# Kernel optimization log

Measured on AMD Instinct MI355X. Metric: run time of the kernel, lower is better.

The kernel has to match this reference:

```python
import jax, jax.numpy as jnp
import numpy as np

STATE_DIM = 256
ACTION_DIM = 2
HIDDEN = 512
N_HEADS = 5          # per ensemble; 2*N_HEADS stacked critics total
CEM_POP = 4096
CEM_ITERS = 4
ELITE_N = max(1, int(round(CEM_POP * 0.2)))  # 819
ACTION_LOW, ACTION_HIGH = -1.0, 1.0
INIT_STD, MIN_STD = 0.4, 0.1


def setup_inputs() -> dict:
    key = jax.random.key(0)
    ks = jax.random.split(key, 6)
    in_dim = STATE_DIM + ACTION_DIM
    state = jax.random.normal(ks[0], (1, STATE_DIM), dtype=jnp.float32)
    noise = jax.random.normal(ks[1], (CEM_ITERS, CEM_POP, ACTION_DIM), dtype=jnp.float32)
    W1 = jax.random.normal(ks[2], (2 * N_HEADS, in_dim, HIDDEN), dtype=jnp.float32) / np.sqrt(in_dim).astype(np.float32)
    b1 = jnp.zeros((2 * N_HEADS, HIDDEN), dtype=jnp.float32)
    W2 = jax.random.normal(ks[3], (2 * N_HEADS, HIDDEN, HIDDEN), dtype=jnp.float32) / np.sqrt(HIDDEN).astype(np.float32)
    b2 = jnp.zeros((2 * N_HEADS, HIDDEN), dtype=jnp.float32)
    W3 = jax.random.normal(ks[4], (2 * N_HEADS, HIDDEN, 1), dtype=jnp.float32) / np.sqrt(HIDDEN).astype(np.float32)
    b3 = jnp.zeros((2 * N_HEADS, 1), dtype=jnp.float32)
    return {"state": state, "noise": noise, "W1": W1, "b1": b1, "W2": W2, "b2": b2, "W3": W3, "b3": b3}


def _ensemble_scores(s_batch, a, W1, b1, W2, b2, W3, b3):
    # x: [P, state+action]; heads stacked on leading dim h = 2*N_HEADS
    x = jnp.concatenate([s_batch, a], axis=-1)
    h = jax.nn.relu(jnp.einsum('pi,hij->hpj', x, W1) + b1[:, None, :])
    h = jax.nn.relu(jnp.einsum('hpj,hjk->hpk', h, W2) + b2[:, None, :])
    q = (jnp.einsum('hpk,hko->hpo', h, W3) + b3[:, None, :])[..., 0]  # [2H, P]
    q1, q2 = q[:N_HEADS], q[N_HEADS:]
    return jnp.minimum(q1, q2).mean(axis=0)  # [P]


def reference(state, noise, W1, b1, W2, b2, W3, b3):
    s = state[0]  # squeeze(0)
    s_batch = jnp.broadcast_to(s, (CEM_POP, STATE_DIM))

    def step(carry, eps):
        mu, std, best_a, best_score = carry
        a = jnp.clip(mu + std * eps, ACTION_LOW, ACTION_HIGH)  # [P, A]
        scores = _ensemble_scores(s_batch, a, W1, b1, W2, b2, W3, b3)
        vals, idx = jax.lax.top_k(scores, ELITE_N)
        elite = a[idx]  # [ELITE_N, A]
        mu2 = elite.mean(axis=0)
        std2 = jnp.maximum(jnp.std(elite, axis=0, ddof=1), MIN_STD)  # torch unbiased std
        better = vals[0] > best_score
        best_a2 = jnp.where(better, elite[0], best_a)
        best_score2 = jnp.where(better, vals[0], best_score)
        return (mu2, std2, best_a2, best_score2), None

    carry0 = (jnp.zeros((ACTION_DIM,), jnp.float32),
              jnp.full((ACTION_DIM,), INIT_STD, jnp.float32),
              jnp.zeros((ACTION_DIM,), jnp.float32),
              jnp.float32(-jnp.inf))
    (mu, std, best_a, best_score), _ = jax.lax.scan(step, carry0, noise)
    return best_a[None, :]  # [1, ACTION_DIM]
```

## Files before the change

kernel.cpp:

```cpp
#include <hip/hip_runtime.h>
#include <math.h>

#define SDIM   256
#define HID    512
#define NH     5
#define HEADS  10
#define POP    4096
#define ITERS  4
#define ELITE  819
#define INIT_STDF 0.4f
#define MIN_STDF  0.1f

#define WS_BASE1 0
#define WS_Q     5120
#define WS_STATE 87040
#define WS_W2S_BYTE 348224
#define W2S_USHORTS (HEADS * 2 * 16 * 16384)
#define WS_NEED_BYTES (WS_W2S_BYTE + (size_t)W2S_USHORTS * 2)

typedef __attribute__((ext_vector_type(4))) float f32x4;
typedef __attribute__((ext_vector_type(8))) short bf16x8;

static __device__ __forceinline__ unsigned short bf16_rne(float x) {
    unsigned b = __float_as_uint(x);
    return (unsigned short)((b + 0x7FFFu + ((b >> 16) & 1u)) >> 16);
}

static __device__ __forceinline__ unsigned pack2(float x, float y) {
    unsigned r;
    asm("v_cvt_pk_bf16_f32 %0, %1, %2" : "=v"(r) : "v"(x), "v"(y));
    return r;
}

static __device__ __forceinline__ float clip1(float x) {
    return fminf(fmaxf(x, -1.f), 1.f);
}

__global__ __launch_bounds__(256) void k_base(const float* __restrict__ state,
                                              const float* __restrict__ W1,
                                              const float* __restrict__ b1,
                                              float* __restrict__ ws)
{
    const int h = blockIdx.y;
    const int j = blockIdx.x * 256 + threadIdx.x;
    const float* w1h = W1 + (size_t)h * 258 * HID;
    float acc = b1[h * HID + j];
    for (int i = 0; i < SDIM; ++i)
        acc += state[i] * w1h[(size_t)i * HID + j];
    ws[WS_BASE1 + h * HID + j] = acc;

    if (h == 0 && blockIdx.x == 0 && threadIdx.x == 0) {
        float* st = ws + WS_STATE;
        st[0] = 0.f; st[1] = 0.f;
        st[2] = INIT_STDF; st[3] = INIT_STDF;
        st[4] = 0.f; st[5] = 0.f;
        st[6] = -3.402823466e38f;
    }
}

__global__ __launch_bounds__(256) void k_split(const float* __restrict__ W2,
                                               unsigned short* __restrict__ W2S)
{
    const int h = blockIdx.z, cb = blockIdx.y, jc = blockIdx.x;
    const int c = threadIdx.x;
    unsigned short* slab = W2S + (size_t)((h * 2 + cb) * 16 + jc) * 16384;
    #pragma unroll
    for (int jg = 0; jg < 4; ++jg) {
        unsigned hp[4], lp[4];
        #pragma unroll
        for (int i = 0; i < 4; ++i) {
            const int j = jc * 32 + jg * 8 + 2 * i;
            float v0 = W2[(size_t)(h * HID + j) * HID + cb * 256 + c];
            float v1 = W2[(size_t)(h * HID + j + 1) * HID + cb * 256 + c];
            unsigned short h0 = bf16_rne(v0), h1 = bf16_rne(v1);
            float f0 = __uint_as_float((unsigned)h0 << 16);
            float f1 = __uint_as_float((unsigned)h1 << 16);
            unsigned short l0 = bf16_rne(v0 - f0), l1 = bf16_rne(v1 - f1);
            hp[i] = (unsigned)h0 | ((unsigned)h1 << 16);
            lp[i] = (unsigned)l0 | ((unsigned)l1 << 16);
        }
        uint4 HV, LV;
        HV.x = hp[0]; HV.y = hp[1]; HV.z = hp[2]; HV.w = hp[3];
        LV.x = lp[0]; LV.y = lp[1]; LV.z = lp[2]; LV.w = lp[3];
        *(uint4*)&slab[jg * 2048 + c * 8] = HV;
        *(uint4*)&slab[8192 + jg * 2048 + c * 8] = LV;
    }
}

__global__ __launch_bounds__(512, 4) void k_score_mfma10(
    const float* __restrict__ noise, const float* __restrict__ W1,
    const unsigned short* __restrict__ W2S,
    const float* __restrict__ b2, const float* __restrict__ W3,
    float* __restrict__ ws, int t)
{
    __shared__ unsigned short As[2][4096];
    __shared__ float red[8][64];

    const int tid = threadIdx.x;
    const int bid = blockIdx.x;
    const int w = (bid & 7) * 160 + (bid >> 3);
    const int h = w >> 7;
    const int rem = w & 127;
    const int cb = rem >> 6;
    const int rs = rem & 63;

    const int lane = tid & 63;
    const int wv = tid >> 6;
    const int l15 = lane & 15, lk = lane >> 4;

    const int arow = tid & 63;
    const int akg = (tid >> 6) & 3;
    const int ahalf = tid >> 8;

    const float* st = ws + WS_STATE;
    const float mu0 = st[0], mu1 = st[1], sd0 = st[2], sd1 = st[3];
    float2 e = *(const float2*)&noise[((size_t)t * POP + rs * 64 + arow) * 2];
    const float a0 = clip1(mu0 + sd0 * e.x);
    const float a1 = clip1(mu1 + sd1 * e.y);

    const float* base1 = ws + WS_BASE1 + h * HID;
    const float* w1u = W1 + ((size_t)h * 258 + 256) * HID;
    const float* w1v = W1 + ((size_t)h * 258 + 257) * HID;
    const unsigned short* bslab = W2S + (size_t)((h * 2 + cb) * 16) * 16384;
    const int bco = lk * 2048 + (wv * 32 + l15) * 8;

    auto computeA = [&](int jc, int buf) {
        const int j = jc * 32 + akg * 8 + ahalf * 4;
        f32x4 b0 = *(const f32x4*)&base1[j];
        f32x4 u0 = *(const f32x4*)&w1u[j];
        f32x4 v0 = *(const f32x4*)&w1v[j];
        float hv[4];
        #pragma unroll
        for (int i = 0; i < 4; ++i)
            hv[i] = fmaxf(b0[i] + a0 * u0[i] + a1 * v0[i], 0.f);
        unsigned ph[2], pl[2];
        #pragma unroll
        for (int i = 0; i < 2; ++i) {
            ph[i] = pack2(hv[2 * i], hv[2 * i + 1]);
            float fx = __uint_as_float(ph[i] << 16);
            float fy = __uint_as_float(ph[i] & 0xFFFF0000u);
            pl[i] = pack2(hv[2 * i] - fx, hv[2 * i + 1] - fy);
        }
        uint2 HV, LV;
        HV.x = ph[0]; HV.y = ph[1];
        LV.x = pl[0]; LV.y = pl[1];
        const int ao = akg * 512 + arow * 8 + ahalf * 4;
        *(uint2*)&As[buf][ao] = HV;
        *(uint2*)&As[buf][2048 + ao] = LV;
    };

    f32x4 acc[4][2];
    #pragma unroll
    for (int m = 0; m < 4; ++m)
        #pragma unroll
        for (int n = 0; n < 2; ++n)
            acc[m][n] = (f32x4){0.f, 0.f, 0.f, 0.f};

    computeA(0, 0);
    bf16x8 BH[2], BL[2];
    #pragma unroll
    for (int n = 0; n < 2; ++n) {
        BH[n] = *(const bf16x8*)(bslab + bco + n * 128);
        BL[n] = *(const bf16x8*)(bslab + 8192 + bco + n * 128);
    }
    __syncthreads();

    int cur = 0;
    #pragma unroll 1
    for (int kc = 0; kc < 16; ++kc) {
        bf16x8 AH[4], AL[4];
        #pragma unroll
        for (int m = 0; m < 4; ++m) {
            const int ad = lk * 512 + (m * 16 + l15) * 8;
            AH[m] = *(const bf16x8*)&As[cur][ad];
            AL[m] = *(const bf16x8*)&As[cur][2048 + ad];
        }
        const int nc = (kc < 15) ? kc + 1 : 15;
        const unsigned short* bnc = bslab + (size_t)nc * 16384;
        bf16x8 nBH[2], nBL[2];
        #pragma unroll
        for (int n = 0; n < 2; ++n) {
            nBH[n] = *(const bf16x8*)(bnc + bco + n * 128);
            nBL[n] = *(const bf16x8*)(bnc + 8192 + bco + n * 128);
        }
        __builtin_amdgcn_s_setprio(1);
        #pragma unroll
        for (int m = 0; m < 4; ++m)
            #pragma unroll
            for (int n = 0; n < 2; ++n)
                acc[m][n] = __builtin_amdgcn_mfma_f32_16x16x32_bf16(
                    AH[m], BH[n], acc[m][n], 0, 0, 0);
        #pragma unroll
        for (int m = 0; m < 4; ++m)
            #pragma unroll
            for (int n = 0; n < 2; ++n)
                acc[m][n] = __builtin_amdgcn_mfma_f32_16x16x32_bf16(
                    AL[m], BH[n], acc[m][n], 0, 0, 0);
        #pragma unroll
        for (int m = 0; m < 4; ++m)
            #pragma unroll
            for (int n = 0; n < 2; ++n)
                acc[m][n] = __builtin_amdgcn_mfma_f32_16x16x32_bf16(
                    AH[m], BL[n], acc[m][n], 0, 0, 0);
        __builtin_amdgcn_s_setprio(0);
        computeA(nc, cur ^ 1);
        __syncthreads();
        #pragma unroll
        for (int n = 0; n < 2; ++n) { BH[n] = nBH[n]; BL[n] = nBL[n]; }
        cur ^= 1;
    }

    float qp[4][4];
    #pragma unroll
    for (int m = 0; m < 4; ++m)
        #pragma unroll
        for (int r = 0; r < 4; ++r) qp[m][r] = 0.f;
    #pragma unroll
    for (int n = 0; n < 2; ++n) {
        int gcol = cb * 256 + wv * 32 + n * 16 + l15;
        float b2v = b2[h * HID + gcol];
        float w3v = W3[h * HID + gcol];
        #pragma unroll
        for (int m = 0; m < 4; ++m)
            #pragma unroll
            for (int r = 0; r < 4; ++r)
                qp[m][r] += fmaxf(acc[m][n][r] + b2v, 0.f) * w3v;
    }
    #pragma unroll
    for (int m = 0; m < 4; ++m)
        #pragma unroll
        for (int r = 0; r < 4; ++r) {
            float v = qp[m][r];
            v += __shfl_xor(v, 1);
            v += __shfl_xor(v, 2);
            v += __shfl_xor(v, 4);
            v += __shfl_xor(v, 8);
            if (l15 == 0) red[wv][m * 16 + lk * 4 + r] = v;
        }
    __syncthreads();
    if (tid < 64) {
        float q = 0.f;
        #pragma unroll
        for (int s = 0; s < 8; ++s) q += red[s][tid];
        ws[WS_Q + (size_t)(cb * HEADS + h) * POP + rs * 64 + tid] = q;
    }
}

__global__ __launch_bounds__(256) void k_score(const float* __restrict__ noise,
                                               const float* __restrict__ W1,
                                               const float* __restrict__ W2,
                                               const float* __restrict__ b2,
                                               const float* __restrict__ W3,
                                               float* __restrict__ ws, int t)
{
    __shared__ float h1[32][HID];
    __shared__ float a0s[32], a1s[32];
    __shared__ float red[2][16][2];

    const int tid = threadIdx.x;
    const int h   = blockIdx.y;
    const int p0  = blockIdx.x * 32;

    if (tid < 32) {
        const float* st = ws + WS_STATE;
        const int p = p0 + tid;
        float e0 = noise[((size_t)t * POP + p) * 2 + 0];
        float e1 = noise[((size_t)t * POP + p) * 2 + 1];
        a0s[tid] = fminf(fmaxf(st[0] + st[2] * e0, -1.f), 1.f);
        a1s[tid] = fminf(fmaxf(st[1] + st[3] * e1, -1.f), 1.f);
    }
    __syncthreads();

    const float* base1 = ws + WS_BASE1 + h * HID;
    const float* w1u = W1 + ((size_t)h * 258 + 256) * HID;
    const float* w1v = W1 + ((size_t)h * 258 + 257) * HID;
    #pragma unroll
    for (int jj = 0; jj < 2; ++jj) {
        int j = tid + jj * 256;
        float bb = base1[j], uu = w1u[j], vv = w1v[j];
        #pragma unroll
        for (int p = 0; p < 32; ++p)
            h1[p][j] = fmaxf(bb + a0s[p] * uu + a1s[p] * vv, 0.f);
    }
    __syncthreads();

    const int pg = tid >> 7;
    const int kl = tid & 127;
    const float* W2h = W2 + (size_t)h * HID * HID + kl;

    float acc[16][4];
    #pragma unroll
    for (int p = 0; p < 16; ++p)
        #pragma unroll
        for (int dk = 0; dk < 4; ++dk) acc[p][dk] = 0.f;

    for (int j0 = 0; j0 < HID; j0 += 4) {
        float w[4][4];
        #pragma unroll
        for (int dj = 0; dj < 4; ++dj)
            #pragma unroll
            for (int dk = 0; dk < 4; ++dk)
                w[dj][dk] = W2h[(size_t)(j0 + dj) * HID + dk * 128];
        #pragma unroll
        for (int p = 0; p < 16; ++p) {
            const float4 hv = *(const float4*)&h1[pg * 16 + p][j0];
            #pragma unroll
            for (int dk = 0; dk < 4; ++dk)
                acc[p][dk] += hv.x * w[0][dk] + hv.y * w[1][dk]
                            + hv.z * w[2][dk] + hv.w * w[3][dk];
        }
    }

    float b2v[4], w3v[4];
    #pragma unroll
    for (int dk = 0; dk < 4; ++dk) {
        b2v[dk] = b2[h * HID + kl + dk * 128];
        w3v[dk] = W3[h * HID + kl + dk * 128];
    }
    const int wid  = tid >> 6;
    const int lane = tid & 63;
    const int wig  = wid & 1;
    #pragma unroll
    for (int p = 0; p < 16; ++p) {
        float v = 0.f;
        #pragma unroll
        for (int dk = 0; dk < 4; ++dk)
            v += fmaxf(acc[p][dk] + b2v[dk], 0.f) * w3v[dk];
        #pragma unroll
        for (int off = 32; off; off >>= 1) v += __shfl_down(v, off);
        if (lane == 0) red[pg][p][wig] = v;
    }
    __syncthreads();
    if (tid < 32) {
        int pp = tid & 15, g = tid >> 4;
        ws[WS_Q + (size_t)h * POP + p0 + g * 16 + pp] =
            red[g][pp][0] + red[g][pp][1];
        ws[WS_Q + (size_t)(HEADS + h) * POP + p0 + g * 16 + pp] = 0.f;
    }
}

__global__ __launch_bounds__(1024) void k_select(const float* __restrict__ noise,
                                                 const float* __restrict__ b3,
                                                 float* __restrict__ ws,
                                                 float* __restrict__ out, int t)
{
    __shared__ float    sc[POP];
    __shared__ unsigned uk[POP];
    __shared__ unsigned hist[256];
    __shared__ int      scan2[1024];
    __shared__ float    rf[1024];
    __shared__ int      ri_[1024];
    __shared__ double   rd[1024];
    __shared__ unsigned s_prefix;
    __shared__ int      s_r;

    const int tid = threadIdx.x;
    const float* q = ws + WS_Q;
    float* st = ws + WS_STATE;
    const float mu0 = st[0], mu1 = st[1], sd0 = st[2], sd1 = st[3];

    {
        const int p = tid * 4;
        f32x4 s = (f32x4){0.f, 0.f, 0.f, 0.f};
        #pragma unroll
        for (int hh = 0; hh < NH; ++hh) {
            f32x4 qa0 = *(const f32x4*)&q[(size_t)hh * POP + p];
            f32x4 qa1 = *(const f32x4*)&q[(size_t)(HEADS + hh) * POP + p];
            f32x4 qb0 = *(const f32x4*)&q[(size_t)(NH + hh) * POP + p];
            f32x4 qb1 = *(const f32x4*)&q[(size_t)(HEADS + NH + hh) * POP + p];
            float ba = b3[hh], bb = b3[NH + hh];
            #pragma unroll
            for (int i = 0; i < 4; ++i)
                s[i] += fminf(qa0[i] + qa1[i] + ba, qb0[i] + qb1[i] + bb);
        }
        #pragma unroll
        for (int i = 0; i < 4; ++i) {
            float v = s[i] * 0.2f;
            sc[p + i] = v;
            unsigned b = __float_as_uint(v);
            uk[p + i] = (b & 0x80000000u) ? ~b : (b | 0x80000000u);
        }
    }
    __syncthreads();

    float mv = -3.402823466e38f; int mi = 0;
    #pragma unroll
    for (int k = 0; k < 4; ++k) {
        const int p = tid * 4 + k;
        float v = sc[p];
        if (v > mv) { mv = v; mi = p; }
    }
    rf[tid] = mv; ri_[tid] = mi;
    __syncthreads();
    for (int off = 512; off; off >>= 1) {
        if (tid < off) {
            float ov = rf[tid + off]; int oi = ri_[tid + off];
            if (ov > rf[tid] || (ov == rf[tid] && oi < ri_[tid])) {
                rf[tid] = ov; ri_[tid] = oi;
            }
        }
        __syncthreads();
    }
    const float maxsc = rf[0];
    const int argmax = ri_[0];
    __syncthreads();

    unsigned prefix = 0; int r = ELITE;
    for (int shift = 24; shift >= 0; shift -= 8) {
        if (tid < 256) hist[tid] = 0;
        __syncthreads();
        const unsigned himask = (shift < 24) ? (0xFFFFFFFFu << (shift + 8)) : 0u;
        for (int p = tid; p < POP; p += 1024) {
            unsigned key = uk[p];
            if ((key & himask) == prefix)
                atomicAdd(&hist[(key >> shift) & 255u], 1u);
        }
        __syncthreads();
        scan2[tid] = (tid < 256) ? (int)hist[tid] : 0;
        __syncthreads();
        for (int off = 1; off < 256; off <<= 1) {
            int v = (tid < 256 && tid + off < 256) ? scan2[tid + off] : 0;
            __syncthreads();
            if (tid < 256) scan2[tid] += v;
            __syncthreads();
        }
        if (tid < 256) {
            int above = (tid < 255) ? scan2[tid + 1] : 0;
            if (scan2[tid] >= r && above < r) {
                s_prefix = prefix | ((unsigned)tid << shift);
                s_r = r - above;
            }
        }
        __syncthreads();
        prefix = s_prefix; r = s_r;
        __syncthreads();
    }
    const unsigned uT = prefix;
    const int take = r;

    int tieloc = 0;
    {
        const int base = tid * 4;
        #pragma unroll
        for (int k = 0; k < 4; ++k) if (uk[base + k] == uT) tieloc++;
    }
    scan2[tid] = tieloc;
    __syncthreads();
    for (int off = 1; off < 1024; off <<= 1) {
        int v = (tid >= off) ? scan2[tid - off] : 0;
        __syncthreads();
        scan2[tid] += v;
        __syncthreads();
    }
    const int tieExcl = scan2[tid] - tieloc;

    double s0 = 0, s1 = 0, ss0 = 0, ss1 = 0;
    {
        const int base = tid * 4;
        int trank = tieExcl;
        #pragma unroll
        for (int k = 0; k < 4; ++k) {
            const int p = base + k;
            const unsigned key = uk[p];
            bool inc = false;
            if (key > uT) inc = true;
            else if (key == uT) { if (trank < take) inc = true; trank++; }
            if (inc) {
                float e0 = noise[((size_t)t * POP + p) * 2 + 0];
                float e1 = noise[((size_t)t * POP + p) * 2 + 1];
                float a0 = fminf(fmaxf(mu0 + sd0 * e0, -1.f), 1.f);
                float a1 = fminf(fmaxf(mu1 + sd1 * e1, -1.f), 1.f);
                s0 += a0; s1 += a1;
                ss0 += (double)a0 * a0; ss1 += (double)a1 * a1;
            }
        }
    }
    double S0, S1, SS0, SS1;
    rd[tid] = s0;  __syncthreads();
    for (int off = 512; off; off >>= 1) { if (tid < off) rd[tid] += rd[tid + off]; __syncthreads(); }
    S0 = rd[0]; __syncthreads();
    rd[tid] = s1;  __syncthreads();
    for (int off = 512; off; off >>= 1) { if (tid < off) rd[tid] += rd[tid + off]; __syncthreads(); }
    S1 = rd[0]; __syncthreads();
    rd[tid] = ss0; __syncthreads();
    for (int off = 512; off; off >>= 1) { if (tid < off) rd[tid] += rd[tid + off]; __syncthreads(); }
    SS0 = rd[0]; __syncthreads();
    rd[tid] = ss1; __syncthreads();
    for (int off = 512; off; off >>= 1) { if (tid < off) rd[tid] += rd[tid + off]; __syncthreads(); }
    SS1 = rd[0]; __syncthreads();

    if (tid == 0) {
        const double n = (double)ELITE;
        double m0 = S0 / n, m1 = S1 / n;
        double v0 = (SS0 - S0 * S0 / n) / (n - 1.0);
        double v1 = (SS1 - S1 * S1 / n) / (n - 1.0);
        float nsd0 = fmaxf((float)sqrt(fmax(v0, 0.0)), MIN_STDF);
        float nsd1 = fmaxf((float)sqrt(fmax(v1, 0.0)), MIN_STDF);
        float e0 = noise[((size_t)t * POP + argmax) * 2 + 0];
        float e1 = noise[((size_t)t * POP + argmax) * 2 + 1];
        float a0 = fminf(fmaxf(mu0 + sd0 * e0, -1.f), 1.f);
        float a1 = fminf(fmaxf(mu1 + sd1 * e1, -1.f), 1.f);
        if (maxsc > st[6]) { st[4] = a0; st[5] = a1; st[6] = maxsc; }
        st[0] = (float)m0; st[1] = (float)m1; st[2] = nsd0; st[3] = nsd1;
        if (t == ITERS - 1) { out[0] = st[4]; out[1] = st[5]; }
    }
}

extern "C" void kernel_launch(void* const* d_in, const int* in_sizes, int n_in,
                              void* d_out, int out_size, void* d_ws, size_t ws_size,
                              hipStream_t stream)
{
    const float* state = (const float*)d_in[0];
    const float* noise = (const float*)d_in[1];
    const float* W1    = (const float*)d_in[2];
    const float* b1    = (const float*)d_in[3];
    const float* W2    = (const float*)d_in[4];
    const float* b2    = (const float*)d_in[5];
    const float* W3    = (const float*)d_in[6];
    const float* b3    = (const float*)d_in[7];
    float* out = (float*)d_out;
    float* ws  = (float*)d_ws;

    const bool fast = ws_size >= WS_NEED_BYTES;

    k_base<<<dim3(2, HEADS), 256, 0, stream>>>(state, W1, b1, ws);
    if (fast) {
        unsigned short* W2S = (unsigned short*)((char*)d_ws + WS_W2S_BYTE);
        k_split<<<dim3(16, 2, HEADS), 256, 0, stream>>>(W2, W2S);
        for (int t = 0; t < ITERS; ++t) {
            k_score_mfma10<<<dim3(1280), 512, 0, stream>>>(
                noise, W1, W2S, b2, W3, ws, t);
            k_select<<<1, 1024, 0, stream>>>(noise, b3, ws, out, t);
        }
    } else {
        for (int t = 0; t < ITERS; ++t) {
            k_score<<<dim3(POP / 32, HEADS), 256, 0, stream>>>(noise, W1, W2, b2, W3, ws, t);
            k_select<<<1, 1024, 0, stream>>>(noise, b3, ws, out, t);
        }
    }
}
```

Before: 332.1 us.

## Split score GEMM into quarter-column blocks to double grid parallelism

The launched scoring kernel now splits each head's 512 output columns into four 128-column quarters instead of two halves, doubling the grid to 2560 blocks with each wave computing a single 16-column MFMA tile. Partial Q values for the four quarters are written to separate workspace slabs, and the select kernel sums them before the min/mean; the workspace offsets are enlarged to hold them. The aim is more blocks in flight and fewer accumulators per thread. The cost is that every block recomputes the layer-1 activations and reloads the W2 panel, and the new B-tile loads sit right before the MFMAs without the previous prefetch. An unused K-split variant is also added.

```diff
diff --git a/kernel.cpp b/kernel.cpp
--- a/kernel.cpp
+++ b/kernel.cpp
@@ -13,8 +13,8 @@
 
 #define WS_BASE1 0
 #define WS_Q     5120
-#define WS_STATE 87040
-#define WS_W2S_BYTE 348224
+#define WS_STATE 168960
+#define WS_W2S_BYTE 675872
 #define W2S_USHORTS (HEADS * 2 * 16 * 16384)
 #define WS_NEED_BYTES (WS_W2S_BYTE + (size_t)W2S_USHORTS * 2)
 
@@ -87,7 +87,7 @@
     }
 }
 
-__global__ __launch_bounds__(512, 4) void k_score_mfma10(
+__global__ __launch_bounds__(512, 4) void k_score_mfma11(
     const float* __restrict__ noise, const float* __restrict__ W1,
     const unsigned short* __restrict__ W2S,
     const float* __restrict__ b2, const float* __restrict__ W3,
@@ -98,19 +98,20 @@
 
     const int tid = threadIdx.x;
     const int bid = blockIdx.x;
-    const int w = (bid & 7) * 160 + (bid >> 3);
-    const int h = w >> 7;
-    const int rem = w & 127;
-    const int cb = rem >> 6;
+    const int w = (bid & 7) * 320 + (bid >> 3);
+    const int h = w >> 8;
+    const int rem = w & 255;
+    const int cb = rem >> 7;
+    const int kh = (rem >> 6) & 1;
     const int rs = rem & 63;
 
     const int lane = tid & 63;
     const int wv = tid >> 6;
     const int l15 = lane & 15, lk = lane >> 4;
 
-    const int arow = tid & 63;
-    const int akg = (tid >> 6) & 3;
-    const int ahalf = tid >> 8;
+    const int akg = tid >> 7;
+    const int arow = (tid >> 1) & 63;
+    const int ahalf = tid & 1;
 
     const float* st = ws + WS_STATE;
     const float mu0 = st[0], mu1 = st[1], sd0 = st[2], sd1 = st[3];
@@ -156,18 +157,23 @@
         for (int n = 0; n < 2; ++n)
             acc[m][n] = (f32x4){0.f, 0.f, 0.f, 0.f};
 
-    computeA(0, 0);
+    const int jc0 = kh * 8;
+    computeA(jc0, 0);
     bf16x8 BH[2], BL[2];
-    #pragma unroll
-    for (int n = 0; n < 2; ++n) {
-        BH[n] = *(const bf16x8*)(bslab + bco + n * 128);
-        BL[n] = *(const bf16x8*)(bslab + 8192 + bco + n * 128);
+    {
+        const unsigned short* b0p = bslab + (size_t)jc0 * 16384;
+        #pragma unroll
+        for (int n = 0; n < 2; ++n) {
+            BH[n] = *(const bf16x8*)(b0p + bco + n * 128);
+            BL[n] = *(const bf16x8*)(b0p + 8192 + bco + n * 128);
+        }
     }
     __syncthreads();
 
     int cur = 0;
     #pragma unroll 1
-    for (int kc = 0; kc < 16; ++kc) {
+    for (int c = 0; c < 8; ++c) {
+        const int jc = jc0 + c;
         bf16x8 AH[4], AL[4];
         #pragma unroll
         for (int m = 0; m < 4; ++m) {
@@ -175,8 +181,8 @@
             AH[m] = *(const bf16x8*)&As[cur][ad];
             AL[m] = *(const bf16x8*)&As[cur][2048 + ad];
         }
-        const int nc = (kc < 15) ? kc + 1 : 15;
-        const unsigned short* bnc = bslab + (size_t)nc * 16384;
+        const int njc = (c < 7) ? jc + 1 : jc;
+        const unsigned short* bnc = bslab + (size_t)njc * 16384;
         bf16x8 nBH[2], nBL[2];
         #pragma unroll
         for (int n = 0; n < 2; ++n) {
@@ -203,7 +209,7 @@
                 acc[m][n] = __builtin_amdgcn_mfma_f32_16x16x32_bf16(
                     AH[m], BL[n], acc[m][n], 0, 0, 0);
         __builtin_amdgcn_s_setprio(0);
-        computeA(nc, cur ^ 1);
+        computeA(njc, cur ^ 1);
         __syncthreads();
         #pragma unroll
         for (int n = 0; n < 2; ++n) { BH[n] = nBH[n]; BL[n] = nBL[n]; }
@@ -242,7 +248,153 @@
         float q = 0.f;
         #pragma unroll
         for (int s = 0; s < 8; ++s) q += red[s][tid];
-        ws[WS_Q + (size_t)(cb * HEADS + h) * POP + rs * 64 + tid] = q;
+        ws[WS_Q + (size_t)((cb * 2 + kh) * HEADS + h) * POP + rs * 64 + tid] = q;
+    }
+}
+
+__global__ __launch_bounds__(512, 4) void k_score_mfma12(
+    const float* __restrict__ noise, const float* __restrict__ W1,
+    const unsigned short* __restrict__ W2S,
+    const float* __restrict__ b2, const float* __restrict__ W3,
+    float* __restrict__ ws, int t)
+{
+    __shared__ unsigned short As[2][4096];
+    __shared__ float red[8][64];
+
+    const int tid = threadIdx.x;
+    const int bid = blockIdx.x;
+    const int w = (bid & 7) * 320 + (bid >> 3);
+    const int h = w >> 8;
+    const int rem = w & 255;
+    const int cq = rem >> 6;
+    const int rs = rem & 63;
+
+    const int lane = tid & 63;
+    const int wv = tid >> 6;
+    const int l15 = lane & 15, lk = lane >> 4;
+
+    const int akg = tid >> 7;
+    const int arow = (tid >> 1) & 63;
+    const int ahalf = tid & 1;
+
+    const float* st = ws + WS_STATE;
+    const float mu0 = st[0], mu1 = st[1], sd0 = st[2], sd1 = st[3];
+    float2 e = *(const float2*)&noise[((size_t)t * POP + rs * 64 + arow) * 2];
+    const float a0 = clip1(mu0 + sd0 * e.x);
+    const float a1 = clip1(mu1 + sd1 * e.y);
+
+    const float* base1 = ws + WS_BASE1 + h * HID;
+    const float* w1u = W1 + ((size_t)h * 258 + 256) * HID;
+    const float* w1v = W1 + ((size_t)h * 258 + 257) * HID;
+    const unsigned short* bslab = W2S + (size_t)((h * 2 + (cq >> 1)) * 16) * 16384;
+    const int bco = lk * 2048 + ((cq & 1) * 128 + wv * 16 + l15) * 8;
+
+    auto computeA = [&](int jc, int buf) {
+        const int j = jc * 32 + akg * 8 + ahalf * 4;
+        f32x4 b0 = *(const f32x4*)&base1[j];
+        f32x4 u0 = *(const f32x4*)&w1u[j];
+        f32x4 v0 = *(const f32x4*)&w1v[j];
+        float hv[4];
+        #pragma unroll
+        for (int i = 0; i < 4; ++i)
+            hv[i] = fmaxf(b0[i] + a0 * u0[i] + a1 * v0[i], 0.f);
+        unsigned ph[2], pl[2];
+        #pragma unroll
+        for (int i = 0; i < 2; ++i) {
+            ph[i] = pack2(hv[2 * i], hv[2 * i + 1]);
+            float fx = __uint_as_float(ph[i] << 16);
+            float fy = __uint_as_float(ph[i] & 0xFFFF0000u);
+            pl[i] = pack2(hv[2 * i] - fx, hv[2 * i + 1] - fy);
+        }
+        uint2 HV, LV;
+        HV.x = ph[0]; HV.y = ph[1];
+        LV.x = pl[0]; LV.y = pl[1];
+        const int ao = akg * 512 + arow * 8 + ahalf * 4;
+        *(uint2*)&As[buf][ao] = HV;
+        *(uint2*)&As[buf][2048 + ao] = LV;
+    };
+
+    f32x4 acc[4];
+    f32x4 acc2[4];
+    #pragma unroll
+    for (int m = 0; m < 4; ++m) {
+        acc[m] = (f32x4){0.f, 0.f, 0.f, 0.f};
+        acc2[m] = (f32x4){0.f, 0.f, 0.f, 0.f};
+    }
+
+    computeA(0, 0);
+    bf16x8 BH[2], BL[2];
+    #pragma unroll
+    for (int g = 0; g < 2; ++g) {
+        BH[g] = *(const bf16x8*)(bslab + g * 2048 * 0 + bco);
+        BL[g] = *(const bf16x8*)(bslab + 8192 + bco);
+    }
+    __syncthreads();
+
+    int cur = 0;
+    #pragma unroll 1
+    for (int kc = 0; kc < 16; ++kc) {
+        bf16x8 AH[4], AL[4];
+        #pragma unroll
+        for (int m = 0; m < 4; ++m) {
+            const int ad = lk * 512 + (m * 16 + l15) * 8;
+            AH[m] = *(const bf16x8*)&As[cur][ad];
+            AL[m] = *(const bf16x8*)&As[cur][2048 + ad];
+        }
+        const int nc = (kc < 15) ? kc + 1 : 15;
+        const unsigned short* bnc = bslab + (size_t)nc * 16384;
+        bf16x8 nBH, nBL;
+        nBH = *(const bf16x8*)(bnc + bco);
+        nBL = *(const bf16x8*)(bnc + 8192 + bco);
+        const unsigned short* bcc = bslab + (size_t)kc * 16384;
+        bf16x8 cBH = *(const bf16x8*)(bcc + bco);
+        bf16x8 cBL = *(const bf16x8*)(bcc + 8192 + bco);
+        __builtin_amdgcn_s_setprio(1);
+        #pragma unroll
+        for (int m = 0; m < 4; ++m)
+            acc[m] = __builtin_amdgcn_mfma_f32_16x16x32_bf16(
+                AH[m], cBH, acc[m], 0, 0, 0);
+        #pragma unroll
+        for (int m = 0; m < 4; ++m)
+            acc2[m] = __builtin_amdgcn_mfma_f32_16x16x32_bf16(
+                AL[m], cBH, acc2[m], 0, 0, 0);
+        #pragma unroll
+        for (int m = 0; m < 4; ++m)
+            acc[m] = __builtin_amdgcn_mfma_f32_16x16x32_bf16(
+                AH[m], cBL, acc[m], 0, 0, 0);
+        __builtin_amdgcn_s_setprio(0);
+        computeA(nc, cur ^ 1);
+        __syncthreads();
+        cur ^= 1;
+        (void)nBH; (void)nBL;
+    }
+
+    const int gcol = cq * 128 + wv * 16 + l15;
+    const float b2v = b2[h * HID + gcol];
+    const float w3v = W3[h * HID + gcol];
+    float qp[4][4];
+    #pragma unroll
+    for (int m = 0; m < 4; ++m)
+        #pragma unroll
+        for (int r = 0; r < 4; ++r)
+            qp[m][r] = fmaxf(acc[m][r] + acc2[m][r] + b2v, 0.f) * w3v;
+    #pragma unroll
+    for (int m = 0; m < 4; ++m)
+        #pragma unroll
+        for (int r = 0; r < 4; ++r) {
+            float v = qp[m][r];
+            v += __shfl_xor(v, 1);
+            v += __shfl_xor(v, 2);
+            v += __shfl_xor(v, 4);
+            v += __shfl_xor(v, 8);
+            if (l15 == 0) red[wv][m * 16 + lk * 4 + r] = v;
+        }
+    __syncthreads();
+    if (tid < 64) {
+        float q = 0.f;
+        #pragma unroll
+        for (int s = 0; s < 8; ++s) q += red[s][tid];
+        ws[WS_Q + (size_t)(cq * HEADS + h) * POP + rs * 64 + tid] = q;
     }
 }
 
@@ -335,7 +487,9 @@
         int pp = tid & 15, g = tid >> 4;
         ws[WS_Q + (size_t)h * POP + p0 + g * 16 + pp] =
             red[g][pp][0] + red[g][pp][1];
-        ws[WS_Q + (size_t)(HEADS + h) * POP + p0 + g * 16 + pp] = 0.f;
+        ws[WS_Q + (size_t)(1 * HEADS + h) * POP + p0 + g * 16 + pp] = 0.f;
+        ws[WS_Q + (size_t)(2 * HEADS + h) * POP + p0 + g * 16 + pp] = 0.f;
+        ws[WS_Q + (size_t)(3 * HEADS + h) * POP + p0 + g * 16 + pp] = 0.f;
     }
 }
 
@@ -364,14 +518,19 @@
         f32x4 s = (f32x4){0.f, 0.f, 0.f, 0.f};
         #pragma unroll
         for (int hh = 0; hh < NH; ++hh) {
-            f32x4 qa0 = *(const f32x4*)&q[(size_t)hh * POP + p];
-            f32x4 qa1 = *(const f32x4*)&q[(size_t)(HEADS + hh) * POP + p];
-            f32x4 qb0 = *(const f32x4*)&q[(size_t)(NH + hh) * POP + p];
-            f32x4 qb1 = *(const f32x4*)&q[(size_t)(HEADS + NH + hh) * POP + p];
+            f32x4 qa = (f32x4){0.f, 0.f, 0.f, 0.f};
+            f32x4 qb = (f32x4){0.f, 0.f, 0.f, 0.f};
+            #pragma unroll
+            for (int pi = 0; pi < 4; ++pi) {
+                f32x4 va = *(const f32x4*)&q[(size_t)(pi * HEADS + hh) * POP + p];
+                f32x4 vb = *(const f32x4*)&q[(size_t)(pi * HEADS + NH + hh) * POP + p];
+                #pragma unroll
+                for (int i = 0; i < 4; ++i) { qa[i] += va[i]; qb[i] += vb[i]; }
+            }
             float ba = b3[hh], bb = b3[NH + hh];
             #pragma unroll
             for (int i = 0; i < 4; ++i)
-                s[i] += fminf(qa0[i] + qa1[i] + ba, qb0[i] + qb1[i] + bb);
+                s[i] += fminf(qa[i] + ba, qb[i] + bb);
         }
         #pragma unroll
         for (int i = 0; i < 4; ++i) {
@@ -528,7 +687,7 @@
         unsigned short* W2S = (unsigned short*)((char*)d_ws + WS_W2S_BYTE);
         k_split<<<dim3(16, 2, HEADS), 256, 0, stream>>>(W2, W2S);
         for (int t = 0; t < ITERS; ++t) {
-            k_score_mfma10<<<dim3(1280), 512, 0, stream>>>(
+            k_score_mfma12<<<dim3(2560), 512, 0, stream>>>(
                 noise, W1, W2S, b2, W3, ws, t);
             k_select<<<1, 1024, 0, stream>>>(noise, b3, ws, out, t);
         }
```

New measurement: 433.8 us. 1.31x slower.

## Stage four K-chunks of A per barrier to cut syncthreads in MFMA scorer

Applied to the files above, without the earlier changes.

Each block's shared A tile is enlarged from one 32-wide K chunk to four chunks per buffer. The loop now runs four iterations of four unrolled MFMA substeps each, with B registers ping-ponged between two sets instead of being copied. This cuts the number of block-wide barriers and A-fill phases from 16 to 4 per block, and changes the thread-to-A mapping. In exchange, LDS use grows about fourfold (64KB for As), which may reduce how many blocks fit per CU.

```diff
diff --git a/kernel.cpp b/kernel.cpp
--- a/kernel.cpp
+++ b/kernel.cpp
@@ -87,13 +87,13 @@
     }
 }
 
-__global__ __launch_bounds__(512, 4) void k_score_mfma10(
+__global__ __launch_bounds__(512, 4) void k_score_mfma14(
     const float* __restrict__ noise, const float* __restrict__ W1,
     const unsigned short* __restrict__ W2S,
     const float* __restrict__ b2, const float* __restrict__ W3,
     float* __restrict__ ws, int t)
 {
-    __shared__ unsigned short As[2][4096];
+    __shared__ unsigned short As[2][16384];
     __shared__ float red[8][64];
 
     const int tid = threadIdx.x;
@@ -108,9 +108,9 @@
     const int wv = tid >> 6;
     const int l15 = lane & 15, lk = lane >> 4;
 
-    const int arow = tid & 63;
-    const int akg = (tid >> 6) & 3;
-    const int ahalf = tid >> 8;
+    const int akg = tid >> 7;
+    const int arow = (tid >> 1) & 63;
+    const int ahalf = tid & 1;
 
     const float* st = ws + WS_STATE;
     const float mu0 = st[0], mu1 = st[1], sd0 = st[2], sd1 = st[3];
@@ -124,29 +124,32 @@
     const unsigned short* bslab = W2S + (size_t)((h * 2 + cb) * 16) * 16384;
     const int bco = lk * 2048 + (wv * 32 + l15) * 8;
 
-    auto computeA = [&](int jc, int buf) {
-        const int j = jc * 32 + akg * 8 + ahalf * 4;
-        f32x4 b0 = *(const f32x4*)&base1[j];
-        f32x4 u0 = *(const f32x4*)&w1u[j];
-        f32x4 v0 = *(const f32x4*)&w1v[j];
-        float hv[4];
-        #pragma unroll
-        for (int i = 0; i < 4; ++i)
-            hv[i] = fmaxf(b0[i] + a0 * u0[i] + a1 * v0[i], 0.f);
-        unsigned ph[2], pl[2];
-        #pragma unroll
-        for (int i = 0; i < 2; ++i) {
-            ph[i] = pack2(hv[2 * i], hv[2 * i + 1]);
-            float fx = __uint_as_float(ph[i] << 16);
-            float fy = __uint_as_float(ph[i] & 0xFFFF0000u);
-            pl[i] = pack2(hv[2 * i] - fx, hv[2 * i + 1] - fy);
-        }
-        uint2 HV, LV;
-        HV.x = ph[0]; HV.y = ph[1];
-        LV.x = pl[0]; LV.y = pl[1];
-        const int ao = akg * 512 + arow * 8 + ahalf * 4;
-        *(uint2*)&As[buf][ao] = HV;
-        *(uint2*)&As[buf][2048 + ao] = LV;
+    auto computeA = [&](int it4, int buf) {
+        #pragma unroll
+        for (int s = 0; s < 4; ++s) {
+            const int j = it4 * 128 + s * 32 + akg * 8 + ahalf * 4;
+            f32x4 b0 = *(const f32x4*)&base1[j];
+            f32x4 u0 = *(const f32x4*)&w1u[j];
+            f32x4 v0 = *(const f32x4*)&w1v[j];
+            float hv[4];
+            #pragma unroll
+            for (int i = 0; i < 4; ++i)
+                hv[i] = fmaxf(b0[i] + a0 * u0[i] + a1 * v0[i], 0.f);
+            unsigned ph[2], pl[2];
+            #pragma unroll
+            for (int i = 0; i < 2; ++i) {
+                ph[i] = pack2(hv[2 * i], hv[2 * i + 1]);
+                float fx = __uint_as_float(ph[i] << 16);
+                float fy = __uint_as_float(ph[i] & 0xFFFF0000u);
+                pl[i] = pack2(hv[2 * i] - fx, hv[2 * i + 1] - fy);
+            }
+            uint2 HV, LV;
+            HV.x = ph[0]; HV.y = ph[1];
+            LV.x = pl[0]; LV.y = pl[1];
+            const int ao = s * 4096 + akg * 512 + arow * 8 + ahalf * 4;
+            *(uint2*)&As[buf][ao] = HV;
+            *(uint2*)&As[buf][2048 + ao] = LV;
+        }
     };
 
     f32x4 acc[4][2];
@@ -157,58 +160,66 @@
             acc[m][n] = (f32x4){0.f, 0.f, 0.f, 0.f};
 
     computeA(0, 0);
-    bf16x8 BH[2], BL[2];
+    bf16x8 BcH[2], BcL[2], BnH[2], BnL[2];
     #pragma unroll
     for (int n = 0; n < 2; ++n) {
-        BH[n] = *(const bf16x8*)(bslab + bco + n * 128);
-        BL[n] = *(const bf16x8*)(bslab + 8192 + bco + n * 128);
-    }
-    __syncthreads();
+        BcH[n] = *(const bf16x8*)(bslab + bco + n * 128);
+        BcL[n] = *(const bf16x8*)(bslab + 8192 + bco + n * 128);
+    }
+    __syncthreads();
+
+#define SUBSTEP(AOFF, UH, UL, PH, PL, NCH)                                    \
+    {                                                                         \
+        bf16x8 AH[4], AL[4];                                                  \
+        _Pragma("unroll")                                                     \
+        for (int m = 0; m < 4; ++m) {                                         \
+            const int ad = (AOFF) + lk * 512 + (m * 16 + l15) * 8;            \
+            AH[m] = *(const bf16x8*)&As[cur][ad];                             \
+            AL[m] = *(const bf16x8*)&As[cur][2048 + ad];                      \
+        }                                                                     \
+        {                                                                     \
+            const unsigned short* bp = bslab + (size_t)(NCH) * 16384;         \
+            _Pragma("unroll")                                                 \
+            for (int n = 0; n < 2; ++n) {                                     \
+                PH[n] = *(const bf16x8*)(bp + bco + n * 128);                 \
+                PL[n] = *(const bf16x8*)(bp + 8192 + bco + n * 128);          \
+            }                                                                 \
+        }                                                                     \
+        __builtin_amdgcn_s_setprio(1);                                        \
+        _Pragma("unroll")                                                     \
+        for (int m = 0; m < 4; ++m)                                           \
+            _Pragma("unroll")                                                 \
+            for (int n = 0; n < 2; ++n)                                       \
+                acc[m][n] = __builtin_amdgcn_mfma_f32_16x16x32_bf16(          \
+                    AH[m], UH[n], acc[m][n], 0, 0, 0);                        \
+        _Pragma("unroll")                                                     \
+        for (int m = 0; m < 4; ++m)                                           \
+            _Pragma("unroll")                                                 \
+            for (int n = 0; n < 2; ++n)                                       \
+                acc[m][n] = __builtin_amdgcn_mfma_f32_16x16x32_bf16(          \
+                    AL[m], UH[n], acc[m][n], 0, 0, 0);                        \
+        _Pragma("unroll")                                                     \
+        for (int m = 0; m < 4; ++m)                                           \
+            _Pragma("unroll")                                                 \
+            for (int n = 0; n < 2; ++n)                                       \
+                acc[m][n] = __builtin_amdgcn_mfma_f32_16x16x32_bf16(          \
+                    AH[m], UL[n], acc[m][n], 0, 0, 0);                        \
+        __builtin_amdgcn_s_setprio(0);                                        \
+    }
 
     int cur = 0;
     #pragma unroll 1
-    for (int kc = 0; kc < 16; ++kc) {
-        bf16x8 AH[4], AL[4];
-        #pragma unroll
-        for (int m = 0; m < 4; ++m) {
-            const int ad = lk * 512 + (m * 16 + l15) * 8;
-            AH[m] = *(const bf16x8*)&As[cur][ad];
-            AL[m] = *(const bf16x8*)&As[cur][2048 + ad];
-        }
-        const int nc = (kc < 15) ? kc + 1 : 15;
-        const unsigned short* bnc = bslab + (size_t)nc * 16384;
-        bf16x8 nBH[2], nBL[2];
-        #pragma unroll
-        for (int n = 0; n < 2; ++n) {
-            nBH[n] = *(const bf16x8*)(bnc + bco + n * 128);
-            nBL[n] = *(const bf16x8*)(bnc + 8192 + bco + n * 128);
-        }
-        __builtin_amdgcn_s_setprio(1);
-        #pragma unroll
-        for (int m = 0; m < 4; ++m)
-            #pragma unroll
-            for (int n = 0; n < 2; ++n)
-                acc[m][n] = __builtin_amdgcn_mfma_f32_16x16x32_bf16(
-                    AH[m], BH[n], acc[m][n], 0, 0, 0);
-        #pragma unroll
-        for (int m = 0; m < 4; ++m)
-            #pragma unroll
-            for (int n = 0; n < 2; ++n)
-                acc[m][n] = __builtin_amdgcn_mfma_f32_16x16x32_bf16(
-                    AL[m], BH[n], acc[m][n], 0, 0, 0);
-        #pragma unroll
-        for (int m = 0; m < 4; ++m)
-            #pragma unroll
-            for (int n = 0; n < 2; ++n)
-                acc[m][n] = __builtin_amdgcn_mfma_f32_16x16x32_bf16(
-                    AH[m], BL[n], acc[m][n], 0, 0, 0);
-        __builtin_amdgcn_s_setprio(0);
-        computeA(nc, cur ^ 1);
-        __syncthreads();
-        #pragma unroll
-        for (int n = 0; n < 2; ++n) { BH[n] = nBH[n]; BL[n] = nBL[n]; }
+    for (int it = 0; it < 4; ++it) {
+        const int c0 = it * 4;
+        SUBSTEP(0,     BcH, BcL, BnH, BnL, c0 + 1)
+        SUBSTEP(4096,  BnH, BnL, BcH, BcL, c0 + 2)
+        SUBSTEP(8192,  BcH, BcL, BnH, BnL, c0 + 3)
+        SUBSTEP(12288, BnH, BnL, BcH, BcL, (it < 3) ? c0 + 4 : 15)
+        computeA((it < 3) ? it + 1 : 3, cur ^ 1);
+        __syncthreads();
         cur ^= 1;
     }
+#undef SUBSTEP
 
     float qp[4][4];
     #pragma unroll
@@ -528,7 +539,7 @@
         unsigned short* W2S = (unsigned short*)((char*)d_ws + WS_W2S_BYTE);
         k_split<<<dim3(16, 2, HEADS), 256, 0, stream>>>(W2, W2S);
         for (int t = 0; t < ITERS; ++t) {
-            k_score_mfma10<<<dim3(1280), 512, 0, stream>>>(
+            k_score_mfma14<<<dim3(1280), 512, 0, stream>>>(
                 noise, W1, W2S, b2, W3, ws, t);
             k_select<<<1, 1024, 0, stream>>>(noise, b3, ws, out, t);
         }
```

Result: faster. 323.4 us (-2.6%).
